# Kernel optimization log

Measured on AMD Instinct MI355X. Metric: run time of the kernel, lower is better.

Reference implementation:

```python
import jax, jax.numpy as jnp
import numpy as np
from jax import lax

KH, KW = 3, 3
C_IN, F = 128, 256
STRIDES = (1, 1)
PADDING = 'VALID'


def setup_inputs() -> dict:
    key = jax.random.key(0)
    k1, k2, k3 = jax.random.split(key, 3)
    inputs = jax.random.normal(k1, (32, 64, 64, C_IN), dtype=jnp.float32)
    # w matches tf.image.extract_patches flattening order: (kh, kw, C) row-major
    w = jax.random.normal(k2, (F, KH * KW * C_IN), dtype=jnp.float32)
    b = jax.random.normal(k3, (F,), dtype=jnp.float32)
    return {"inputs": inputs, "w": w, "b": b}


def reference(inputs, w, b):
    # w: (F, kh*kw*C) flattened in (kh, kw, C) order -> HWIO kernel (kh, kw, C, F).
    # The original does patches (N,Ho,Wo,P) * w (F,P) broadcast then sum over P,
    # which is exactly a VALID 2D convolution; express it as a real conv.
    kernel = w.reshape(F, KH, KW, C_IN).transpose(1, 2, 3, 0)
    out = lax.conv_general_dilated(
        inputs, kernel,
        window_strides=STRIDES,
        padding=PADDING,
        dimension_numbers=('NHWC', 'HWIO', 'NHWC'),
    )
    return out + b  # (N, Ho, Wo, F)
```

## Files before the change

kernel.cpp:

```cpp
#include <hip/hip_runtime.h>

typedef __attribute__((ext_vector_type(8))) short bf16x8;
typedef __attribute__((ext_vector_type(4))) float f32x4;

#define GLOAD_LDS16(gp, lp)                                                   \
  __builtin_amdgcn_global_load_lds(                                           \
      (const __attribute__((address_space(1))) void*)(gp),                    \
      (__attribute__((address_space(3))) void*)(lp), 16, 0, 0)

__device__ inline unsigned short f2bf(float f) {
  union { float f; unsigned u; } a; a.f = f;
  unsigned u = a.u;
  return (unsigned short)((u + 0x7fffu + ((u >> 16) & 1u)) >> 16);
}

__global__ void cvt_f32_bf16(const float* __restrict__ in,
                             unsigned short* __restrict__ out, int n4) {
  int i = blockIdx.x * blockDim.x + threadIdx.x;
  int stride = gridDim.x * blockDim.x;
  for (; i < n4; i += stride) {
    float4 v = reinterpret_cast<const float4*>(in)[i];
    ushort4 o;
    o.x = f2bf(v.x); o.y = f2bf(v.y); o.z = f2bf(v.z); o.w = f2bf(v.w);
    reinterpret_cast<ushort4*>(out)[i] = o;
  }
}

#define BM 128
#define BK 64

__global__ __launch_bounds__(512) void conv_gemm(
    const unsigned short* __restrict__ A,
    const unsigned short* __restrict__ Bw,
    const float* __restrict__ bias,
    float* __restrict__ out)
{
  __shared__ unsigned short sA[BM * BK];
  __shared__ unsigned short sB[256 * BK];

  const int tid = threadIdx.x;
  const int bm = blockIdx.x;

  const int r0 = tid >> 3;
  const int s  = tid & 7;
  const int sp = s ^ (r0 & 7);

  int m0 = bm * BM + r0;
  int m1 = m0 + 64;
  int n0 = m0 / 3844, rem0 = m0 % 3844;
  int n1 = m1 / 3844, rem1 = m1 % 3844;
  const int p0 = (n0 * 64 + rem0 / 62) * 64 + rem0 % 62;
  const int p1 = (n1 * 64 + rem1 / 62) * 64 + rem1 % 62;

  const int wv   = tid >> 6;
  const int lane = tid & 63;
  const int wm   = wv >> 2;
  const int wn   = wv & 3;
  const int l15  = lane & 15;
  const int lhi  = lane >> 4;

  f32x4 acc[4][4];
  #pragma unroll
  for (int i = 0; i < 4; ++i)
    #pragma unroll
    for (int j = 0; j < 4; ++j)
      acc[i][j] = (f32x4){0.f, 0.f, 0.f, 0.f};

  for (int step = 0; step < 18; ++step) {
    const int pos = step >> 1;
    const int kh = pos / 3, kw = pos % 3;
    const int c0 = (step & 1) << 6;
    const int dpix = kh * 64 + kw;

    __syncthreads();

    {
      const unsigned short* g0 = A + (size_t)(p0 + dpix) * 128 + c0 + sp * 8;
      const unsigned short* g1 = A + (size_t)(p1 + dpix) * 128 + c0 + sp * 8;
      GLOAD_LDS16(g0, &sA[tid * 8]);
      GLOAD_LDS16(g1, &sA[(tid + 512) * 8]);
    }
    {
      const int dk = pos * 128 + c0 + sp * 8;
      #pragma unroll
      for (int it = 0; it < 4; ++it) {
        const int f = it * 64 + r0;
        GLOAD_LDS16(Bw + (size_t)f * 1152 + dk, &sB[(it * 512 + tid) * 8]);
      }
    }
    __syncthreads();

    #pragma unroll
    for (int kk = 0; kk < 2; ++kk) {
      const int t = kk * 4 + lhi;
      bf16x8 af[4], bfr[4];
      #pragma unroll
      for (int i = 0; i < 4; ++i) {
        const int row = wm * 64 + i * 16 + l15;
        af[i] = *reinterpret_cast<const bf16x8*>(
            reinterpret_cast<const char*>(sA) + row * 128 + ((t ^ (row & 7)) * 16));
      }
      #pragma unroll
      for (int j = 0; j < 4; ++j) {
        const int fl = wn * 64 + j * 16 + l15;
        bfr[j] = *reinterpret_cast<const bf16x8*>(
            reinterpret_cast<const char*>(sB) + fl * 128 + ((t ^ (fl & 7)) * 16));
      }
      #pragma unroll
      for (int i = 0; i < 4; ++i)
        #pragma unroll
        for (int j = 0; j < 4; ++j)
          acc[i][j] = __builtin_amdgcn_mfma_f32_16x16x32_bf16(af[i], bfr[j],
                                                              acc[i][j], 0, 0, 0);
    }
  }

  const int colb = wn * 64 + l15;
  #pragma unroll
  for (int j = 0; j < 4; ++j) {
    const float bv = bias[colb + j * 16];
    #pragma unroll
    for (int i = 0; i < 4; ++i) {
      const int rowb = bm * BM + wm * 64 + i * 16 + lhi * 4;
      #pragma unroll
      for (int r = 0; r < 4; ++r)
        out[(size_t)(rowb + r) * 256 + colb + j * 16] = acc[i][j][r] + bv;
    }
  }
}

extern "C" void kernel_launch(void* const* d_in, const int* in_sizes, int n_in,
                              void* d_out, int out_size, void* d_ws, size_t ws_size,
                              hipStream_t stream) {
  const float* inp = (const float*)d_in[0];
  const float* w   = (const float*)d_in[1];
  const float* b   = (const float*)d_in[2];
  float* out = (float*)d_out;

  unsigned short* wsA = (unsigned short*)d_ws;
  unsigned short* wsB = wsA + 16777216;

  cvt_f32_bf16<<<2048, 256, 0, stream>>>(inp, wsA, 16777216 / 4);
  cvt_f32_bf16<<<288, 256, 0, stream>>>(w, wsB, 294912 / 4);
  conv_gemm<<<961, 512, 0, stream>>>(wsA, wsB, b, out);
}
```

Measured before the change: 262.7 us.

## Double-buffer implicit-GEMM conv with 256-row tiles and interleaved load/MFMA phases

Doubles the output tile to 256 rows by 256 filters per block and splits the K loop into half-steps of 32 channels. Global-to-LDS loads go into a two-buffer scheme with explicit vmcnt waits, barriers and MFMA priority raising, so the next tiles load while the current ones compute. The goal is to hide global load latency and reuse each B fragment across more rows. In exchange it uses 128KB of LDS and twice the accumulator registers, launches only 481 blocks, and needs clamped row indices with a bounds check on the last block.

Result: slower. 275.7 us (+5.0%).

```diff
diff --git a/kernel.cpp b/kernel.cpp
--- a/kernel.cpp
+++ b/kernel.cpp
@@ -26,105 +26,150 @@
   }
 }
 
-#define BM 128
-#define BK 64
+#define M_TOT 123008
 
-__global__ __launch_bounds__(512) void conv_gemm(
+#define OFFS(tau, oA, oB) do {                                                \
+    int _tap = (tau) >> 1; int _kh = (_tap * 11) >> 5; int _kw = _tap - _kh * 3; \
+    oA = (_kh * 64 + _kw) * 128 + ((tau) & 1) * 64;                           \
+    oB = _tap * 128 + ((tau) & 1) * 64;                                       \
+  } while (0)
+
+__global__ __launch_bounds__(512, 2) void conv_gemm(
     const unsigned short* __restrict__ A,
     const unsigned short* __restrict__ Bw,
     const float* __restrict__ bias,
     float* __restrict__ out)
 {
-  __shared__ unsigned short sA[BM * BK];
-  __shared__ unsigned short sB[256 * BK];
+  __shared__ char lds[131072] __attribute__((aligned(16)));
 
   const int tid = threadIdx.x;
   const int bm = blockIdx.x;
 
-  const int r0 = tid >> 3;
-  const int s  = tid & 7;
-  const int sp = s ^ (r0 & 7);
-
-  int m0 = bm * BM + r0;
-  int m1 = m0 + 64;
+  const int r0 = tid >> 2;
+  const int sp = (tid & 3) ^ ((tid >> 3) & 3);
+  int m0 = bm * 256 + r0;        if (m0 > M_TOT - 1) m0 = M_TOT - 1;
+  int m1 = bm * 256 + r0 + 128;  if (m1 > M_TOT - 1) m1 = M_TOT - 1;
   int n0 = m0 / 3844, rem0 = m0 % 3844;
   int n1 = m1 / 3844, rem1 = m1 % 3844;
   const int p0 = (n0 * 64 + rem0 / 62) * 64 + rem0 % 62;
   const int p1 = (n1 * 64 + rem1 / 62) * 64 + rem1 % 62;
+  const int gA0 = p0 * 128 + sp * 8;
+  const int gA1 = p1 * 128 + sp * 8;
+  const int gB0 = r0 * 1152 + sp * 8;
+  const int gB1 = gB0 + 128 * 1152;
 
-  const int wv   = tid >> 6;
-  const int lane = tid & 63;
-  const int wm   = wv >> 2;
-  const int wn   = wv & 3;
-  const int l15  = lane & 15;
-  const int lhi  = lane >> 4;
+  const int lane = tid & 63, wv = tid >> 6;
+  const int wm = wv >> 2, wn = wv & 3;
+  const int l15 = lane & 15, s = lane >> 4;
+  const int rbA = wm * 128 + l15;
+  const int pA = rbA * 64 + ((s ^ ((rbA >> 1) & 3)) * 16);
+  const int rbB = wn * 64 + l15;
+  const int pB = 32768 + rbB * 64 + ((s ^ ((rbB >> 1) & 3)) * 16);
 
-  f32x4 acc[4][4];
+#define LDSA(bufp, i_, kk)                                                    \
+  (*reinterpret_cast<const bf16x8*>(lds + (bufp) * 65536 + (kk) * 16384 + pA + (i_) * 1024))
+#define LDSB(bufp, j_, kk)                                                    \
+  (*reinterpret_cast<const bf16x8*>(lds + (bufp) * 65536 + (kk) * 16384 + pB + (j_) * 1024))
+
+#define STAGE_A(bufp, kk, offA) do {                                          \
+    GLOAD_LDS16(A + gA0 + (offA) + (kk) * 32,                                 \
+                lds + (bufp) * 65536 + (kk) * 16384 + tid * 16);              \
+    GLOAD_LDS16(A + gA1 + (offA) + (kk) * 32,                                 \
+                lds + (bufp) * 65536 + (kk) * 16384 + (tid + 512) * 16);      \
+  } while (0)
+#define STAGE_B(bufp, kk, offB) do {                                          \
+    GLOAD_LDS16(Bw + gB0 + (offB) + (kk) * 32,                                \
+                lds + (bufp) * 65536 + 32768 + (kk) * 16384 + tid * 16);      \
+    GLOAD_LDS16(Bw + gB1 + (offB) + (kk) * 32,                                \
+                lds + (bufp) * 65536 + 32768 + (kk) * 16384 + (tid + 512) * 16); \
+  } while (0)
+
+  f32x4 acc[8][4];
   #pragma unroll
-  for (int i = 0; i < 4; ++i)
+  for (int i = 0; i < 8; ++i)
     #pragma unroll
     for (int j = 0; j < 4; ++j)
       acc[i][j] = (f32x4){0.f, 0.f, 0.f, 0.f};
 
-  for (int step = 0; step < 18; ++step) {
-    const int pos = step >> 1;
-    const int kh = pos / 3, kw = pos % 3;
-    const int c0 = (step & 1) << 6;
-    const int dpix = kh * 64 + kw;
+  bf16x8 bk[4];
 
-    __syncthreads();
+#define PHASE(bufp, kk, rbase, readb, STAGE_STMT, dofence) do {               \
+    bf16x8 af[4];                                                             \
+    if (readb) {                                                              \
+      _Pragma("unroll") for (int j = 0; j < 4; ++j) bk[j] = LDSB(bufp, j, kk);\
+    }                                                                         \
+    _Pragma("unroll") for (int ii = 0; ii < 4; ++ii)                          \
+      af[ii] = LDSA(bufp, (rbase) + ii, kk);                                  \
+    STAGE_STMT;                                                               \
+    if (dofence) {                                                            \
+      asm volatile("s_waitcnt vmcnt(6)" ::: "memory");                        \
+      __builtin_amdgcn_sched_barrier(0);                                      \
+    }                                                                         \
+    __builtin_amdgcn_s_barrier();                                             \
+    __builtin_amdgcn_s_setprio(1);                                            \
+    _Pragma("unroll") for (int ii = 0; ii < 4; ++ii)                          \
+      _Pragma("unroll") for (int j = 0; j < 4; ++j)                           \
+        acc[(rbase) + ii][j] = __builtin_amdgcn_mfma_f32_16x16x32_bf16(       \
+            af[ii], bk[j], acc[(rbase) + ii][j], 0, 0, 0);                    \
+    __builtin_amdgcn_s_setprio(0);                                            \
+    __builtin_amdgcn_s_barrier();                                             \
+    if (dofence) __builtin_amdgcn_sched_barrier(0);                           \
+  } while (0)
 
-    {
-      const unsigned short* g0 = A + (size_t)(p0 + dpix) * 128 + c0 + sp * 8;
-      const unsigned short* g1 = A + (size_t)(p1 + dpix) * 128 + c0 + sp * 8;
-      GLOAD_LDS16(g0, &sA[tid * 8]);
-      GLOAD_LDS16(g1, &sA[(tid + 512) * 8]);
-    }
-    {
-      const int dk = pos * 128 + c0 + sp * 8;
-      #pragma unroll
-      for (int it = 0; it < 4; ++it) {
-        const int f = it * 64 + r0;
-        GLOAD_LDS16(Bw + (size_t)f * 1152 + dk, &sB[(it * 512 + tid) * 8]);
-      }
-    }
-    __syncthreads();
+  {
+    int oA0, oB0, oA1, oB1;
+    OFFS(0, oA0, oB0); OFFS(1, oA1, oB1);
+    STAGE_B(0, 0, oB0); STAGE_A(0, 0, oA0); STAGE_B(0, 1, oB0); STAGE_A(0, 1, oA0);
+    STAGE_B(1, 0, oB1); STAGE_A(1, 0, oA1); STAGE_B(1, 1, oB1);
+    asm volatile("s_waitcnt vmcnt(6)" ::: "memory");
+    __builtin_amdgcn_s_barrier();
+    __builtin_amdgcn_sched_barrier(0);
+  }
 
-    #pragma unroll
-    for (int kk = 0; kk < 2; ++kk) {
-      const int t = kk * 4 + lhi;
-      bf16x8 af[4], bfr[4];
-      #pragma unroll
-      for (int i = 0; i < 4; ++i) {
-        const int row = wm * 64 + i * 16 + l15;
-        af[i] = *reinterpret_cast<const bf16x8*>(
-            reinterpret_cast<const char*>(sA) + row * 128 + ((t ^ (row & 7)) * 16));
-      }
-      #pragma unroll
-      for (int j = 0; j < 4; ++j) {
-        const int fl = wn * 64 + j * 16 + l15;
-        bfr[j] = *reinterpret_cast<const bf16x8*>(
-            reinterpret_cast<const char*>(sB) + fl * 128 + ((t ^ (fl & 7)) * 16));
-      }
-      #pragma unroll
-      for (int i = 0; i < 4; ++i)
-        #pragma unroll
-        for (int j = 0; j < 4; ++j)
-          acc[i][j] = __builtin_amdgcn_mfma_f32_16x16x32_bf16(af[i], bfr[j],
-                                                              acc[i][j], 0, 0, 0);
-    }
+  #pragma unroll 1
+  for (int it = 0; it < 9; ++it) {
+    const int t1 = 2 * it + 1;
+    const int t2 = (2 * it + 2 > 17) ? 17 : 2 * it + 2;
+    const int t3 = (2 * it + 3 > 17) ? 17 : 2 * it + 3;
+    int oA1, oB1, oA2, oB2, oA3, oB3;
+    OFFS(t1, oA1, oB1); OFFS(t2, oA2, oB2); OFFS(t3, oA3, oB3);
+
+    PHASE(0, 0, 0, 1, STAGE_A(1, 1, oA1), 0);
+    PHASE(0, 0, 4, 0, STAGE_B(0, 0, oB2), 0);
+    PHASE(0, 1, 0, 1, STAGE_A(0, 0, oA2), 0);
+    PHASE(0, 1, 4, 0, STAGE_B(0, 1, oB2), 1);
+    PHASE(1, 0, 0, 1, STAGE_A(0, 1, oA2), 0);
+    PHASE(1, 0, 4, 0, STAGE_B(1, 0, oB3), 0);
+    PHASE(1, 1, 0, 1, STAGE_A(1, 0, oA3), 0);
+    PHASE(1, 1, 4, 0, STAGE_B(1, 1, oB3), 1);
   }
 
   const int colb = wn * 64 + l15;
-  #pragma unroll
-  for (int j = 0; j < 4; ++j) {
-    const float bv = bias[colb + j * 16];
+  const int rbase = bm * 256 + wm * 128 + s * 4;
+  if (bm != 480) {
     #pragma unroll
-    for (int i = 0; i < 4; ++i) {
-      const int rowb = bm * BM + wm * 64 + i * 16 + lhi * 4;
+    for (int j = 0; j < 4; ++j) {
+      const float bv = bias[colb + j * 16];
       #pragma unroll
-      for (int r = 0; r < 4; ++r)
-        out[(size_t)(rowb + r) * 256 + colb + j * 16] = acc[i][j][r] + bv;
+      for (int ii = 0; ii < 8; ++ii) {
+        #pragma unroll
+        for (int r = 0; r < 4; ++r)
+          out[(size_t)(rbase + ii * 16 + r) * 256 + colb + j * 16] = acc[ii][j][r] + bv;
+      }
+    }
+  } else {
+    #pragma unroll
+    for (int j = 0; j < 4; ++j) {
+      const float bv = bias[colb + j * 16];
+      #pragma unroll
+      for (int ii = 0; ii < 8; ++ii) {
+        #pragma unroll
+        for (int r = 0; r < 4; ++r) {
+          const int row = rbase + ii * 16 + r;
+          if (row < M_TOT)
+            out[(size_t)row * 256 + colb + j * 16] = acc[ii][j][r] + bv;
+        }
+      }
     }
   }
 }
@@ -142,5 +187,5 @@
 
   cvt_f32_bf16<<<2048, 256, 0, stream>>>(inp, wsA, 16777216 / 4);
   cvt_f32_bf16<<<288, 256, 0, stream>>>(w, wsB, 294912 / 4);
-  conv_gemm<<<961, 512, 0, stream>>>(wsA, wsB, b, out);
+  conv_gemm<<<481, 512, 0, stream>>>(wsA, wsB, b, out);
 }
```

## Double-buffer A tiles, preload fragment-ordered B into registers, remap blocks per XCD

Applied to the files above, without the earlier changes.

The weights are pre-permuted into MFMA fragment order so each wave loads its B fragments straight from global into registers, and only the A tile goes through LDS, double-buffered with partial vmcnt waits. Blocks shrink to 256 threads, with each wave owning all 128 rows and 64 filters, and two blocks may share a CU. Block indices are remapped so each XCD gets a contiguous range of M tiles for better L2 locality. The aim is to overlap global loads with MFMA work and drop the B LDS traffic and the double barrier per step, at the cost of more registers per thread and a hand-tuned wait count.

After: 267.0 us. No clear change (+1.7%).

```diff
diff --git a/kernel.cpp b/kernel.cpp
--- a/kernel.cpp
+++ b/kernel.cpp
@@ -26,105 +26,143 @@
   }
 }
 
-#define BM 128
-#define BK 64
+__global__ void prep_B(const float* __restrict__ w,
+                       unsigned short* __restrict__ Bp) {
+  const int id = blockIdx.x * blockDim.x + threadIdx.x;
+  const int lane = id & 63, frag = id >> 6;
+  const int tau32 = frag >> 4, fgrp = frag & 15;
+  const int row = fgrp * 16 + (lane & 15);
+  const int k0 = tau32 * 32 + ((lane >> 4) << 3);
+  const float* src = w + row * 1152 + k0;
+  float4 v0 = reinterpret_cast<const float4*>(src)[0];
+  float4 v1 = reinterpret_cast<const float4*>(src)[1];
+  ushort4 o0, o1;
+  o0.x = f2bf(v0.x); o0.y = f2bf(v0.y); o0.z = f2bf(v0.z); o0.w = f2bf(v0.w);
+  o1.x = f2bf(v1.x); o1.y = f2bf(v1.y); o1.z = f2bf(v1.z); o1.w = f2bf(v1.w);
+  reinterpret_cast<ushort4*>(Bp)[id * 2] = o0;
+  reinterpret_cast<ushort4*>(Bp)[id * 2 + 1] = o1;
+}
 
-__global__ __launch_bounds__(512) void conv_gemm(
+__global__ __launch_bounds__(256, 2) void conv_gemm(
     const unsigned short* __restrict__ A,
-    const unsigned short* __restrict__ Bw,
+    const unsigned short* __restrict__ Bp,
     const float* __restrict__ bias,
     float* __restrict__ out)
 {
-  __shared__ unsigned short sA[BM * BK];
-  __shared__ unsigned short sB[256 * BK];
+  __shared__ char lds[32768] __attribute__((aligned(16)));
+  const int tid = threadIdx.x;
 
-  const int tid = threadIdx.x;
-  const int bm = blockIdx.x;
+  const int bid = blockIdx.x;
+  const int xcd = bid & 7, idx = bid >> 3;
+  const int bm = (xcd == 0) ? idx : (121 + (xcd - 1) * 120 + idx);
 
-  const int r0 = tid >> 3;
-  const int s  = tid & 7;
-  const int sp = s ^ (r0 & 7);
+  const int srow = tid >> 2;
+  const int sp = (tid & 3) ^ ((tid >> 3) & 3);
+  const int m0 = bm * 128 + srow;
+  const int m1 = m0 + 64;
+  const int n0 = m0 / 3844, q0 = m0 % 3844;
+  const int n1 = m1 / 3844, q1 = m1 % 3844;
+  const int p_lo = (n0 * 64 + q0 / 62) * 64 + q0 % 62;
+  const int p_hi = (n1 * 64 + q1 / 62) * 64 + q1 % 62;
 
-  int m0 = bm * BM + r0;
-  int m1 = m0 + 64;
-  int n0 = m0 / 3844, rem0 = m0 % 3844;
-  int n1 = m1 / 3844, rem1 = m1 % 3844;
-  const int p0 = (n0 * 64 + rem0 / 62) * 64 + rem0 % 62;
-  const int p1 = (n1 * 64 + rem1 / 62) * 64 + rem1 % 62;
+#define STAGE_A(bufbase, aoff) do {                                           \
+    GLOAD_LDS16(A + (size_t)p_lo * 128 + (aoff) + sp * 8,                     \
+                lds + (bufbase) + tid * 16);                                  \
+    GLOAD_LDS16(A + (size_t)p_hi * 128 + (aoff) + sp * 8,                     \
+                lds + (bufbase) + 4096 + tid * 16);                           \
+    GLOAD_LDS16(A + (size_t)p_lo * 128 + (aoff) + 32 + sp * 8,                \
+                lds + (bufbase) + 8192 + tid * 16);                           \
+    GLOAD_LDS16(A + (size_t)p_hi * 128 + (aoff) + 32 + sp * 8,                \
+                lds + (bufbase) + 8192 + 4096 + tid * 16);                    \
+  } while (0)
 
-  const int wv   = tid >> 6;
   const int lane = tid & 63;
-  const int wm   = wv >> 2;
-  const int wn   = wv & 3;
-  const int l15  = lane & 15;
-  const int lhi  = lane >> 4;
+  const int wn = tid >> 6;
+  const int l15 = lane & 15, s = lane >> 4;
+  const int rdoff = l15 * 64 + ((s ^ ((l15 >> 1) & 3)) * 16);
+  const bf16x8* bB = reinterpret_cast<const bf16x8*>(Bp) + wn * 256 + lane;
 
-  f32x4 acc[4][4];
+#define BPRE(bb, tau) do {                                                    \
+    _Pragma("unroll") for (int j = 0; j < 4; ++j) {                           \
+      bb[j * 2]     = bB[(tau) * 2048 + j * 64];                              \
+      bb[j * 2 + 1] = bB[(tau) * 2048 + 1024 + j * 64];                       \
+    }                                                                         \
+  } while (0)
+
+  f32x4 acc[8][4];
   #pragma unroll
-  for (int i = 0; i < 4; ++i)
+  for (int i = 0; i < 8; ++i)
     #pragma unroll
     for (int j = 0; j < 4; ++j)
       acc[i][j] = (f32x4){0.f, 0.f, 0.f, 0.f};
 
-  for (int step = 0; step < 18; ++step) {
-    const int pos = step >> 1;
-    const int kh = pos / 3, kw = pos % 3;
-    const int c0 = (step & 1) << 6;
-    const int dpix = kh * 64 + kw;
+  bf16x8 b0[8], b1[8];
 
-    __syncthreads();
+#define COMPUTE(bufbase, bb) do {                                             \
+    _Pragma("unroll")                                                         \
+    for (int kk = 0; kk < 2; ++kk) {                                          \
+      __builtin_amdgcn_s_setprio(1);                                         \
+      _Pragma("unroll")                                                       \
+      for (int i = 0; i < 8; ++i) {                                           \
+        bf16x8 af = *reinterpret_cast<const bf16x8*>(                         \
+            lds + (bufbase) + kk * 8192 + rdoff + i * 1024);                  \
+        acc[i][0] = __builtin_amdgcn_mfma_f32_16x16x32_bf16(af, bb[0 + kk],   \
+                                                            acc[i][0], 0,0,0);\
+        acc[i][1] = __builtin_amdgcn_mfma_f32_16x16x32_bf16(af, bb[2 + kk],   \
+                                                            acc[i][1], 0,0,0);\
+        acc[i][2] = __builtin_amdgcn_mfma_f32_16x16x32_bf16(af, bb[4 + kk],   \
+                                                            acc[i][2], 0,0,0);\
+        acc[i][3] = __builtin_amdgcn_mfma_f32_16x16x32_bf16(af, bb[6 + kk],   \
+                                                            acc[i][3], 0,0,0);\
+      }                                                                       \
+      __builtin_amdgcn_s_setprio(0);                                         \
+    }                                                                         \
+  } while (0)
 
-    {
-      const unsigned short* g0 = A + (size_t)(p0 + dpix) * 128 + c0 + sp * 8;
-      const unsigned short* g1 = A + (size_t)(p1 + dpix) * 128 + c0 + sp * 8;
-      GLOAD_LDS16(g0, &sA[tid * 8]);
-      GLOAD_LDS16(g1, &sA[(tid + 512) * 8]);
-    }
-    {
-      const int dk = pos * 128 + c0 + sp * 8;
-      #pragma unroll
-      for (int it = 0; it < 4; ++it) {
-        const int f = it * 64 + r0;
-        GLOAD_LDS16(Bw + (size_t)f * 1152 + dk, &sB[(it * 512 + tid) * 8]);
-      }
-    }
-    __syncthreads();
+#define FENCE() do {                                                          \
+    asm volatile("s_waitcnt vmcnt(20)" ::: "memory");                         \
+    __builtin_amdgcn_sched_barrier(0);                                        \
+    __builtin_amdgcn_s_barrier();                                             \
+  } while (0)
 
-    #pragma unroll
-    for (int kk = 0; kk < 2; ++kk) {
-      const int t = kk * 4 + lhi;
-      bf16x8 af[4], bfr[4];
-      #pragma unroll
-      for (int i = 0; i < 4; ++i) {
-        const int row = wm * 64 + i * 16 + l15;
-        af[i] = *reinterpret_cast<const bf16x8*>(
-            reinterpret_cast<const char*>(sA) + row * 128 + ((t ^ (row & 7)) * 16));
-      }
-      #pragma unroll
-      for (int j = 0; j < 4; ++j) {
-        const int fl = wn * 64 + j * 16 + l15;
-        bfr[j] = *reinterpret_cast<const bf16x8*>(
-            reinterpret_cast<const char*>(sB) + fl * 128 + ((t ^ (fl & 7)) * 16));
-      }
-      #pragma unroll
-      for (int i = 0; i < 4; ++i)
-        #pragma unroll
-        for (int j = 0; j < 4; ++j)
-          acc[i][j] = __builtin_amdgcn_mfma_f32_16x16x32_bf16(af[i], bfr[j],
-                                                              acc[i][j], 0, 0, 0);
-    }
+#define AOFF(tau, dst) do {                                                   \
+    int _tap = (tau) >> 1; int _kh = (_tap * 11) >> 5; int _kw = _tap - _kh * 3; \
+    dst = (_kh * 64 + _kw) * 128 + ((tau) & 1) * 64;                          \
+  } while (0)
+
+  STAGE_A(0, 0);
+  BPRE(b0, 0);
+
+  #pragma unroll 1
+  for (int t = 0; t < 9; ++t) {
+    const int t1 = 2 * t + 1;
+    const int t2 = (2 * t + 2 > 17) ? 17 : (2 * t + 2);
+    int aoff1, aoff2;
+    AOFF(t1, aoff1); AOFF(t2, aoff2);
+
+    STAGE_A(16384, aoff1);
+    BPRE(b1, t1);
+    FENCE();
+    COMPUTE(0, b0);
+    __builtin_amdgcn_s_barrier();
+
+    STAGE_A(0, aoff2);
+    BPRE(b0, t2);
+    FENCE();
+    COMPUTE(16384, b1);
+    __builtin_amdgcn_s_barrier();
   }
 
   const int colb = wn * 64 + l15;
+  const int rb = bm * 128 + s * 4;
   #pragma unroll
   for (int j = 0; j < 4; ++j) {
     const float bv = bias[colb + j * 16];
     #pragma unroll
-    for (int i = 0; i < 4; ++i) {
-      const int rowb = bm * BM + wm * 64 + i * 16 + lhi * 4;
+    for (int i = 0; i < 8; ++i) {
       #pragma unroll
       for (int r = 0; r < 4; ++r)
-        out[(size_t)(rowb + r) * 256 + colb + j * 16] = acc[i][j][r] + bv;
+        out[(size_t)(rb + i * 16 + r) * 256 + colb + j * 16] = acc[i][j][r] + bv;
     }
   }
 }
@@ -141,6 +179,6 @@
   unsigned short* wsB = wsA + 16777216;
 
   cvt_f32_bf16<<<2048, 256, 0, stream>>>(inp, wsA, 16777216 / 4);
-  cvt_f32_bf16<<<288, 256, 0, stream>>>(w, wsB, 294912 / 4);
-  conv_gemm<<<961, 512, 0, stream>>>(wsA, wsB, b, out);
+  prep_B<<<144, 256, 0, stream>>>(w, wsB);
+  conv_gemm<<<961, 256, 0, stream>>>(wsA, wsB, b, out);
 }
```
